# Performance work log

Measured on AMD Instinct MI355X. Metric: run time of the kernel, lower is better.

## Reference

```python
import jax, jax.numpy as jnp
import numpy as np

NEG_ATT = 0.2   # GATv2Conv internal leaky_relu slope
NEG_ACT = 0.01  # nn.LeakyReLU default slope (activation between layers)

def _segment_softmax(logits, seg, n):
    m = jax.ops.segment_max(logits, seg, num_segments=n)
    ex = jnp.exp(logits - m[seg])
    s = jax.ops.segment_sum(ex, seg, num_segments=n)
    return ex / s[seg]

def _gatv2(h, Wl, bl, Wr, br, att, bias, src, dst, n):
    # PyG GATv2Conv, heads=1: xl = lin_l(h) (source/message), xr = lin_r(h) (target)
    xl = h @ Wl + bl                                   # [N, H]
    xr = h @ Wr + br                                   # [N, H]
    e = jax.nn.leaky_relu(xl[src] + xr[dst], NEG_ATT)  # [E, H]
    logits = e @ att                                   # [E]
    alpha = _segment_softmax(logits, dst, n)           # softmax over incoming edges per dst
    out = jax.ops.segment_sum(xl[src] * alpha[:, None], dst, num_segments=n)
    return out + bias

def setup_inputs() -> dict:
    key = jax.random.key(0)
    G, P, DEG, DIN, H, EX, OUT, NC = 4096, 24, 8, 32, 128, 8, 3, 6
    N = G * P
    E = N * DEG
    ks = jax.random.split(key, 16)
    x = jax.random.normal(ks[0], (N, DIN), jnp.float32)
    gid = jnp.arange(E) // (P * DEG)  # edges stay within their graph
    src = gid * P + jax.random.randint(ks[1], (E,), 0, P)
    dst = gid * P + jax.random.randint(ks[2], (E,), 0, P)
    batch = jnp.repeat(jnp.arange(G), P)
    extra_feat = jax.random.normal(ks[3], (G, EX), jnp.float32)
    sc = lambda k, shp: jax.random.normal(k, shp, jnp.float32) * 0.05
    return dict(
        x=x, src=src, dst=dst, batch=batch, extra_feat=extra_feat,
        W_init0=sc(ks[4], (DIN, H)), b_init0=jnp.zeros((H,), jnp.float32),
        W_init1=sc(ks[5], (H, H)), b_init1=jnp.zeros((H,), jnp.float32),
        Wl=sc(ks[6], (NC, H, H)), bl=jnp.zeros((NC, H), jnp.float32),
        Wr=sc(ks[7], (NC, H, H)), br=jnp.zeros((NC, H), jnp.float32),
        att=sc(ks[8], (NC, H)), cbias=jnp.zeros((NC, H), jnp.float32),
        Wf0=sc(ks[9], (H + EX, H)), bf0=jnp.zeros((H,), jnp.float32),
        Wf1=sc(ks[10], (H, H)), bf1=jnp.zeros((H,), jnp.float32),
        Wf2=sc(ks[11], (H, OUT)), bf2=jnp.zeros((OUT,), jnp.float32),
    )

def reference(x, src, dst, batch, extra_feat,
              W_init0, b_init0, W_init1, b_init1,
              Wl, bl, Wr, br, att, cbias,
              Wf0, bf0, Wf1, bf1, Wf2, bf2):
    N = x.shape[0]
    G = extra_feat.shape[0]
    # init MLP
    h = jax.nn.leaky_relu(x @ W_init0 + b_init0, NEG_ACT)
    h = jax.nn.leaky_relu(h @ W_init1 + b_init1, NEG_ACT)
    # GATv2Conv adds self-loops
    loop = jnp.arange(N)
    src_sl = jnp.concatenate([src, loop])
    dst_sl = jnp.concatenate([dst, loop])
    NUM_GAT, MP = 2, 3
    for g in range(NUM_GAT):
        for m in range(MP):
            c = g * MP + m
            h = _gatv2(h, Wl[c], bl[c], Wr[c], br[c], att[c], cbias[c], src_sl, dst_sl, N)
            if m < MP - 1:  # BasicGNN: act between convs, not after last
                h = jax.nn.leaky_relu(h, NEG_ACT)
    # global_add_pool + extra features + final MLP
    pooled = jax.ops.segment_sum(h, batch, num_segments=G)
    z = jnp.concatenate([pooled, extra_feat], axis=1)
    z = jax.nn.leaky_relu(z @ Wf0 + bf0, NEG_ACT)
    z = jax.nn.leaky_relu(z @ Wf1 + bf1, NEG_ACT)
    return z @ Wf2 + bf2
```

## Files before the change

### kernel.cpp

```cpp
#include <hip/hip_runtime.h>

#define NG   4096
#define P    24
#define EPG  192
#define ESL  216
#define DIN  32
#define H    128
#define EX   8
#define NOUT 3
#define HSS  136
#define XTS  36
#define AMS  36

typedef _Float16 f16x8 __attribute__((ext_vector_type(8)));
typedef _Float16 h2    __attribute__((ext_vector_type(2)));
typedef float    f32x4 __attribute__((ext_vector_type(4)));

__device__ __forceinline__ unsigned short f2h(float v) {
    _Float16 h = (_Float16)v; unsigned short u; __builtin_memcpy(&u, &h, 2); return u;
}
__device__ __forceinline__ float h2f(unsigned short u) {
    _Float16 h; __builtin_memcpy(&h, &u, 2); return (float)h;
}
__device__ __forceinline__ unsigned pkadd(unsigned a, unsigned b) {
    h2 x, y; __builtin_memcpy(&x, &a, 4); __builtin_memcpy(&y, &b, 4);
    h2 z = x + y; unsigned r; __builtin_memcpy(&r, &z, 4); return r;
}
__device__ __forceinline__ float lrelu(float v, float s) { return v > 0.f ? v : v * s; }

#define STPAIR(BASE, ROW, COL, VAL)                                           \
    do {                                                                      \
        unsigned o_ = (unsigned)__builtin_amdgcn_mov_dpp(                     \
            (int)(unsigned)(VAL), 0xB1, 0xF, 0xF, true);                      \
        if (!(lane & 1))                                                      \
            *reinterpret_cast<unsigned*>(&(BASE)[(ROW) * HSS + (COL)]) =      \
                (unsigned)(VAL) | (o_ << 16);                                 \
    } while (0)

__global__ void cvtw(const float* __restrict__ W0, const float* __restrict__ W1,
                     const float* __restrict__ Wl, const float* __restrict__ Wr,
                     const float* __restrict__ att, const float* __restrict__ bl,
                     const float* __restrict__ br, unsigned short* __restrict__ ws) {
    int i = blockIdx.x * 256 + threadIdx.x;
    if (i < 217088) {
        float v;
        if (i < 4096)        { int n = i >> 5, k = i & 31;  v = W0[k * 128 + n]; }
        else if (i < 20480)  { int j = i - 4096;  int n = j >> 7, k = j & 127; v = W1[k * 128 + n]; }
        else if (i < 118784) { int j = i - 20480; int c = j >> 14, r = j & 16383;
                               int n = r >> 7, k = r & 127; v = Wl[c * 16384 + k * 128 + n]; }
        else                 { int j = i - 118784; int c = j >> 14, r = j & 16383;
                               int n = r >> 7, k = r & 127; v = Wr[c * 16384 + k * 128 + n]; }
        ws[i] = f2h(v);
    } else if (i < 241664) {
        int j = i - 217088;
        const float* W = (j < 12288) ? Wl : Wr;
        if (j >= 12288) j -= 12288;
        int c = j >> 11, r = j & 2047, row = r >> 7, k = r & 127;
        float v = 0.f;
        if (row == 0) {
            for (int q = 0; q < 128; ++q) v += W[c * 16384 + k * 128 + q] * att[c * 128 + q];
        }
        ws[i] = f2h(v);
    } else if (i < 241676) {
        int c = i - 241664;
        const float* B = (c < 6) ? bl : br;
        int cc = (c < 6) ? c : c - 6;
        float s = 0.f;
        for (int q = 0; q < 128; ++q) s += B[cc * 128 + q] * att[cc * 128 + q];
        ((float*)(ws + 241664))[c] = s;
    }
}

__global__ __launch_bounds__(256, 4) void gat_all(
    const float* __restrict__ x,
    const int*   __restrict__ src,
    const int*   __restrict__ dst,
    const float* __restrict__ extra,
    const float* __restrict__ b0,  const float* __restrict__ b1,
    const float* __restrict__ bl,  const float* __restrict__ br,
    const float* __restrict__ att, const float* __restrict__ cbias,
    const float* __restrict__ Wf0, const float* __restrict__ bf0,
    const float* __restrict__ Wf1, const float* __restrict__ bf1,
    const float* __restrict__ Wf2, const float* __restrict__ bf2,
    const unsigned short* __restrict__ wsb,
    float* __restrict__ out)
{
    __shared__ __align__(16) unsigned char LDSM[32768];
    unsigned short* hb  = (unsigned short*)(LDSM);
    unsigned short* xlb = (unsigned short*)(LDSM + 6528);
    unsigned short* xrb = (unsigned short*)(LDSM + 13056);
    unsigned short* xlT = (unsigned short*)(LDSM + 19584);
    float*          Am  = (float*)(LDSM + 28800);
    float*          sn  = (float*)(LDSM + 32256);
    unsigned int*   ath = (unsigned int*)(LDSM + 32512);

    const int g    = blockIdx.x;
    const int t    = threadIdx.x;
    const int lane = t & 63;
    const int w    = t >> 6;
    const int m16  = lane & 15;
    const int kc   = lane >> 4;
    const long long gn = (long long)g * P;

    const unsigned short* W0T = wsb;
    const unsigned short* W1T = wsb + 4096;
    const unsigned short* WLT = wsb + 20480;
    const unsigned short* WRT = wsb + 118784;
    const float* wsf = (const float*)(wsb + 241664);

    int s_e = 0, d_e = 0;
    if (t < ESL) {
        if (t < EPG) {
            s_e = src[(long long)g * EPG + t] - (int)gn;
            d_e = dst[(long long)g * EPG + t] - (int)gn;
        } else { s_e = d_e = t - EPG; }
    }

    if (t < 192) {
        float4 v = *reinterpret_cast<const float4*>(&x[gn * DIN + t * 4]);
        int n = t >> 3, k = (t & 7) * 4;
        *reinterpret_cast<ushort4*>(&xlT[n * XTS + k]) =
            make_ushort4(f2h(v.x), f2h(v.y), f2h(v.z), f2h(v.w));
    } else {
        int u = t - 192;
        int r = 24 + (u >> 3), k = (u & 7) * 4;
        *reinterpret_cast<ushort4*>(&xlT[r * XTS + k]) = make_ushort4(0, 0, 0, 0);
    }
    __syncthreads();

    {
        f32x4 acc[4] = {};
        f16x8 a = *reinterpret_cast<const f16x8*>(&xlT[((w & 1) * 16 + m16) * XTS + kc * 8]);
        #pragma unroll
        for (int i = 0; i < 4; ++i) {
            int nt = (w >> 1) * 4 + i;
            f16x8 b = *reinterpret_cast<const f16x8*>(&W0T[(nt * 16 + m16) * 32 + kc * 8]);
            acc[i] = __builtin_amdgcn_mfma_f32_16x16x32_f16(a, b, acc[i], 0, 0, 0);
        }
        const bool live = !((w & 1) && kc >= 2);
        if (live) {
            #pragma unroll
            for (int i = 0; i < 4; ++i) {
                int col = (w >> 1) * 64 + i * 16 + m16;
                float bv = b0[col];
                #pragma unroll
                for (int r = 0; r < 4; ++r) {
                    int row = (w & 1) * 16 + kc * 4 + r;
                    unsigned short ub = f2h(lrelu(acc[i][r] + bv, 0.01f));
                    STPAIR(xlb, row, col, ub);
                }
            }
        }
    }
    __syncthreads();

    {
        unsigned* xz = reinterpret_cast<unsigned*>(xlT);
        #pragma unroll
        for (int i = 0; i < 9; ++i) xz[t + i * 256] = 0u;
        f32x4 acc[4] = {};
        for (int kt = 0; kt < 4; ++kt) {
            f16x8 a = *reinterpret_cast<const f16x8*>(&xlb[((w & 1) * 16 + m16) * HSS + kt * 32 + kc * 8]);
            #pragma unroll
            for (int i = 0; i < 4; ++i) {
                int nt = (w >> 1) * 4 + i;
                f16x8 b = *reinterpret_cast<const f16x8*>(&W1T[(nt * 16 + m16) * 128 + kt * 32 + kc * 8]);
                acc[i] = __builtin_amdgcn_mfma_f32_16x16x32_f16(a, b, acc[i], 0, 0, 0);
            }
        }
        const bool live = !((w & 1) && kc >= 2);
        if (live) {
            #pragma unroll
            for (int i = 0; i < 4; ++i) {
                int col = (w >> 1) * 64 + i * 16 + m16;
                float bv = b1[col];
                #pragma unroll
                for (int r = 0; r < 4; ++r) {
                    int row = (w & 1) * 16 + kc * 4 + r;
                    unsigned short ub = f2h(lrelu(acc[i][r] + bv, 0.01f));
                    STPAIR(hb, row, col, ub);
                }
            }
        }
    }
    __syncthreads();

    for (int c = 0; c < 6; ++c) {
        if (t < ESL) *reinterpret_cast<float4*>(&Am[t * 4]) = make_float4(0.f, 0.f, 0.f, 0.f);
        if (t < 64) ath[t] = ((unsigned)f2h(att[c * H + 2 * t])) |
                             (((unsigned)f2h(att[c * H + 2 * t + 1])) << 16);

        const unsigned short* WT   = ((w & 1) ? WRT : WLT) + c * 16384;
        const unsigned short* WAX  = wsb + 217088 + ((w & 1) ? 12288 : 0) + c * 2048;
        const float*          bias = ((w & 1) ? br : bl) + c * H;
        f32x4 acc[8] = {};
        f32x4 acce[2] = {};
        for (int kt = 0; kt < 4; ++kt) {
            f16x8 a0 = *reinterpret_cast<const f16x8*>(&hb[(m16)      * HSS + kt * 32 + kc * 8]);
            f16x8 a1 = *reinterpret_cast<const f16x8*>(&hb[(16 + m16) * HSS + kt * 32 + kc * 8]);
            #pragma unroll
            for (int i = 0; i < 4; ++i) {
                int nt = (w >> 1) * 4 + i;
                f16x8 b = *reinterpret_cast<const f16x8*>(&WT[(nt * 16 + m16) * 128 + kt * 32 + kc * 8]);
                acc[i]     = __builtin_amdgcn_mfma_f32_16x16x32_f16(a0, b, acc[i],     0, 0, 0);
                acc[4 + i] = __builtin_amdgcn_mfma_f32_16x16x32_f16(a1, b, acc[4 + i], 0, 0, 0);
            }
            if (w >= 2) {
                f16x8 bx = *reinterpret_cast<const f16x8*>(&WAX[m16 * 128 + kt * 32 + kc * 8]);
                acce[0] = __builtin_amdgcn_mfma_f32_16x16x32_f16(a0, bx, acce[0], 0, 0, 0);
                acce[1] = __builtin_amdgcn_mfma_f32_16x16x32_f16(a1, bx, acce[1], 0, 0, 0);
            }
        }
        {
            unsigned short* XO = (w & 1) ? xrb : xlb;
            const bool isL = !(w & 1);
            #pragma unroll
            for (int mt = 0; mt < 2; ++mt) {
                const bool live = !(mt == 1 && kc >= 2);
                if (live) {
                    #pragma unroll
                    for (int i = 0; i < 4; ++i) {
                        int col = (w >> 1) * 64 + i * 16 + m16;
                        float bv = bias[col];
                        unsigned short ub[4];
                        #pragma unroll
                        for (int r = 0; r < 4; ++r) {
                            int row = mt * 16 + kc * 4 + r;
                            ub[r] = f2h(acc[mt * 4 + i][r] + bv);
                            STPAIR(XO, row, col, ub[r]);
                        }
                        if (isL)
                            *reinterpret_cast<ushort4*>(&xlT[col * XTS + mt * 16 + kc * 4]) =
                                make_ushort4(ub[0], ub[1], ub[2], ub[3]);
                    }
                }
            }
            if (w >= 2 && m16 == 0) {
                float cst = (w == 2) ? wsf[c] : wsf[6 + c];
                float* dp = (w == 2) ? sn : (sn + 32);
                #pragma unroll
                for (int mt = 0; mt < 2; ++mt)
                #pragma unroll
                for (int r = 0; r < 4; ++r)
                    dp[mt * 16 + kc * 4 + r] = acce[mt][r] + cst;
            }
        }
        __syncthreads();

        if (t < ESL) {
            const uint4* xa = reinterpret_cast<const uint4*>(&xlb[s_e * HSS]);
            const uint4* xb = reinterpret_cast<const uint4*>(&xrb[d_e * HSS]);
            const uint4* ap = reinterpret_cast<const uint4*>(ath);
            float a0 = 0.f, a1 = 0.f, a2 = 0.f, a3 = 0.f;
            #pragma unroll 4
            for (int cc = 0; cc < 16; ++cc) {
                uint4 wa = xa[cc], wb = xb[cc], pp = ap[cc];
                unsigned u0 = pkadd(wa.x, wb.x) & 0x7fff7fffu;
                unsigned u1 = pkadd(wa.y, wb.y) & 0x7fff7fffu;
                unsigned u2 = pkadd(wa.z, wb.z) & 0x7fff7fffu;
                unsigned u3 = pkadd(wa.w, wb.w) & 0x7fff7fffu;
                asm volatile("v_dot2_f32_f16 %0, %1, %2, %0" : "+v"(a0) : "v"(u0), "v"(pp.x));
                asm volatile("v_dot2_f32_f16 %0, %1, %2, %0" : "+v"(a1) : "v"(u1), "v"(pp.y));
                asm volatile("v_dot2_f32_f16 %0, %1, %2, %0" : "+v"(a2) : "v"(u2), "v"(pp.z));
                asm volatile("v_dot2_f32_f16 %0, %1, %2, %0" : "+v"(a3) : "v"(u3), "v"(pp.w));
            }
            float abss = (a0 + a1) + (a2 + a3);
            float lg = fmaf(0.6f, sn[s_e] + sn[32 + d_e], 0.4f * abss);
            atomicAdd(&Am[d_e * AMS + s_e], __expf(lg));
        }
        __syncthreads();

        {
            int arow = (w & 1) * 16 + m16;
            float4 u0, u1;
            if (arow < P) {
                u0 = *reinterpret_cast<const float4*>(&Am[arow * AMS + kc * 8]);
                u1 = *reinterpret_cast<const float4*>(&Am[arow * AMS + kc * 8 + 4]);
            } else {
                u0 = make_float4(0.f, 0.f, 0.f, 0.f);
                u1 = u0;
            }
            float rs = u0.x + u0.y + u0.z + u0.w + u1.x + u1.y + u1.z + u1.w;
            rs += __shfl_xor(rs, 16);
            rs += __shfl_xor(rs, 32);
            float sc = (arow < P) ? __builtin_amdgcn_rcpf(rs) : 0.f;
            f16x8 a;
            a[0] = (_Float16)(u0.x * sc); a[1] = (_Float16)(u0.y * sc);
            a[2] = (_Float16)(u0.z * sc); a[3] = (_Float16)(u0.w * sc);
            a[4] = (_Float16)(u1.x * sc); a[5] = (_Float16)(u1.y * sc);
            a[6] = (_Float16)(u1.z * sc); a[7] = (_Float16)(u1.w * sc);
            f32x4 acc2[4] = {};
            #pragma unroll
            for (int i = 0; i < 4; ++i) {
                int nt = (w >> 1) * 4 + i;
                f16x8 b = *reinterpret_cast<const f16x8*>(&xlT[(nt * 16 + m16) * XTS + kc * 8]);
                acc2[i] = __builtin_amdgcn_mfma_f32_16x16x32_f16(a, b, acc2[i], 0, 0, 0);
            }
            const bool doact = (c % 3) < 2;
            const bool live = !((w & 1) && kc >= 2);
            if (live) {
                #pragma unroll
                for (int i = 0; i < 4; ++i) {
                    int col = (w >> 1) * 64 + i * 16 + m16;
                    float cb = cbias[c * H + col];
                    #pragma unroll
                    for (int r = 0; r < 4; ++r) {
                        int row = (w & 1) * 16 + kc * 4 + r;
                        float v = acc2[i][r] + cb;
                        if (doact) v = lrelu(v, 0.01f);
                        unsigned short ub = f2h(v);
                        STPAIR(hb, row, col, ub);
                    }
                }
            }
        }
        __syncthreads();
    }

    float* scr = (float*)(LDSM + 6528);
    float* z  = scr;
    float* pa = scr + 144;
    float* pb = scr + 288;
    float* h1 = scr + 432;
    float* qa = scr + 576;
    float* qb = scr + 720;
    float* h2 = scr + 864;
    if (t < H) {
        float s = 0.f;
        for (int r = 0; r < P; ++r) s += h2f(hb[r * HSS + t]);
        z[t] = s;
    } else if (t < H + EX) {
        z[t] = extra[(long long)g * EX + (t - H)];
    }
    __syncthreads();
    {
        int j = t & 127, half = t >> 7;
        float a = half ? 0.f : bf0[j];
        int k0 = half ? 68 : 0, k1 = half ? 136 : 68;
        for (int k = k0; k < k1; ++k) a += z[k] * Wf0[k * H + j];
        (half ? pb : pa)[j] = a;
    }
    __syncthreads();
    if (t < H) h1[t] = lrelu(pa[t] + pb[t], 0.01f);
    __syncthreads();
    {
        int j = t & 127, half = t >> 7;
        float a = half ? 0.f : bf1[j];
        int k0 = half * 64, k1 = k0 + 64;
        for (int k = k0; k < k1; ++k) a += h1[k] * Wf1[k * H + j];
        (half ? qb : qa)[j] = a;
    }
    __syncthreads();
    if (t < H) h2[t] = lrelu(qa[t] + qb[t], 0.01f);
    __syncthreads();
    if (t < NOUT) {
        float a = bf2[t];
        for (int k = 0; k < H; ++k) a += h2[k] * Wf2[k * NOUT + t];
        out[(long long)g * NOUT + t] = a;
    }
}

extern "C" void kernel_launch(void* const* d_in, const int* in_sizes, int n_in,
                              void* d_out, int out_size, void* d_ws, size_t ws_size,
                              hipStream_t stream) {
    (void)in_sizes; (void)n_in; (void)out_size; (void)ws_size;
    const float* x     = (const float*)d_in[0];
    const int*   src   = (const int*)  d_in[1];
    const int*   dst   = (const int*)  d_in[2];
    const float* extra = (const float*)d_in[4];
    const float* W0    = (const float*)d_in[5];
    const float* b0    = (const float*)d_in[6];
    const float* W1    = (const float*)d_in[7];
    const float* b1    = (const float*)d_in[8];
    const float* Wl    = (const float*)d_in[9];
    const float* bl    = (const float*)d_in[10];
    const float* Wr    = (const float*)d_in[11];
    const float* br    = (const float*)d_in[12];
    const float* att   = (const float*)d_in[13];
    const float* cbias = (const float*)d_in[14];
    const float* Wf0   = (const float*)d_in[15];
    const float* bf0   = (const float*)d_in[16];
    const float* Wf1   = (const float*)d_in[17];
    const float* bf1   = (const float*)d_in[18];
    const float* Wf2   = (const float*)d_in[19];
    const float* bf2   = (const float*)d_in[20];
    unsigned short* wsb = (unsigned short*)d_ws;
    float* out = (float*)d_out;

    cvtw<<<945, 256, 0, stream>>>(W0, W1, Wl, Wr, att, bl, br, wsb);
    gat_all<<<NG, 256, 0, stream>>>(x, src, dst, extra, b0, b1, bl, br, att, cbias,
                                    Wf0, bf0, Wf1, bf1, Wf2, bf2, wsb, out);
}
```

Before: 380.2 us.

## Double block size to 512 threads and redistribute MFMA tiles across eight waves

Raises the per-graph block from 256 to 512 threads (8 waves) and remaps every MFMA stage so each wave computes fewer output column tiles: the init MLP layers, the Wl/Wr projections (now 2 column tiles per wave) and the attention-weighted aggregation. The goal is more wave-level parallelism per graph and lower per-wave serial MFMA chains and register pressure. In exchange it adds waves that share the same LDS and barriers, duplicates A-fragment loads across waves, and may reduce the number of resident blocks per CU. The final MLP stages are guarded to keep using only the first 256 threads.

```diff
diff --git a/kernel.cpp b/kernel.cpp
--- a/kernel.cpp
+++ b/kernel.cpp
@@ -71,7 +71,7 @@
     }
 }
 
-__global__ __launch_bounds__(256, 4) void gat_all(
+__global__ __launch_bounds__(512, 4) void gat_all(
     const float* __restrict__ x,
     const int*   __restrict__ src,
     const int*   __restrict__ dst,
@@ -121,7 +121,7 @@
         int n = t >> 3, k = (t & 7) * 4;
         *reinterpret_cast<ushort4*>(&xlT[n * XTS + k]) =
             make_ushort4(f2h(v.x), f2h(v.y), f2h(v.z), f2h(v.w));
-    } else {
+    } else if (t < 256) {
         int u = t - 192;
         int r = 24 + (u >> 3), k = (u & 7) * 4;
         *reinterpret_cast<ushort4*>(&xlT[r * XTS + k]) = make_ushort4(0, 0, 0, 0);
@@ -129,26 +129,23 @@
     __syncthreads();
 
     {
-        f32x4 acc[4] = {};
-        f16x8 a = *reinterpret_cast<const f16x8*>(&xlT[((w & 1) * 16 + m16) * XTS + kc * 8]);
-        #pragma unroll
-        for (int i = 0; i < 4; ++i) {
-            int nt = (w >> 1) * 4 + i;
-            f16x8 b = *reinterpret_cast<const f16x8*>(&W0T[(nt * 16 + m16) * 32 + kc * 8]);
-            acc[i] = __builtin_amdgcn_mfma_f32_16x16x32_f16(a, b, acc[i], 0, 0, 0);
-        }
-        const bool live = !((w & 1) && kc >= 2);
-        if (live) {
-            #pragma unroll
-            for (int i = 0; i < 4; ++i) {
-                int col = (w >> 1) * 64 + i * 16 + m16;
-                float bv = b0[col];
-                #pragma unroll
-                for (int r = 0; r < 4; ++r) {
-                    int row = (w & 1) * 16 + kc * 4 + r;
-                    unsigned short ub = f2h(lrelu(acc[i][r] + bv, 0.01f));
-                    STPAIR(xlb, row, col, ub);
-                }
+        f16x8 b = *reinterpret_cast<const f16x8*>(&W0T[(w * 16 + m16) * 32 + kc * 8]);
+        f32x4 acc[2] = {};
+        #pragma unroll
+        for (int mt = 0; mt < 2; ++mt) {
+            f16x8 a = *reinterpret_cast<const f16x8*>(&xlT[(mt * 16 + m16) * XTS + kc * 8]);
+            acc[mt] = __builtin_amdgcn_mfma_f32_16x16x32_f16(a, b, acc[mt], 0, 0, 0);
+        }
+        int col = w * 16 + m16;
+        float bv = b0[col];
+        #pragma unroll
+        for (int mt = 0; mt < 2; ++mt) {
+            if (mt == 1 && kc >= 2) continue;
+            #pragma unroll
+            for (int r = 0; r < 4; ++r) {
+                int row = mt * 16 + kc * 4 + r;
+                unsigned short ub = f2h(lrelu(acc[mt][r] + bv, 0.01f));
+                STPAIR(xlb, row, col, ub);
             }
         }
     }
@@ -157,29 +154,28 @@
     {
         unsigned* xz = reinterpret_cast<unsigned*>(xlT);
         #pragma unroll
-        for (int i = 0; i < 9; ++i) xz[t + i * 256] = 0u;
-        f32x4 acc[4] = {};
+        for (int i = 0; i < 4; ++i) xz[t + i * 512] = 0u;
+        if (t < 256) xz[2048 + t] = 0u;
+        f32x4 acc[2] = {};
+        #pragma unroll
         for (int kt = 0; kt < 4; ++kt) {
-            f16x8 a = *reinterpret_cast<const f16x8*>(&xlb[((w & 1) * 16 + m16) * HSS + kt * 32 + kc * 8]);
-            #pragma unroll
-            for (int i = 0; i < 4; ++i) {
-                int nt = (w >> 1) * 4 + i;
-                f16x8 b = *reinterpret_cast<const f16x8*>(&W1T[(nt * 16 + m16) * 128 + kt * 32 + kc * 8]);
-                acc[i] = __builtin_amdgcn_mfma_f32_16x16x32_f16(a, b, acc[i], 0, 0, 0);
-            }
-        }
-        const bool live = !((w & 1) && kc >= 2);
-        if (live) {
-            #pragma unroll
-            for (int i = 0; i < 4; ++i) {
-                int col = (w >> 1) * 64 + i * 16 + m16;
-                float bv = b1[col];
-                #pragma unroll
-                for (int r = 0; r < 4; ++r) {
-                    int row = (w & 1) * 16 + kc * 4 + r;
-                    unsigned short ub = f2h(lrelu(acc[i][r] + bv, 0.01f));
-                    STPAIR(hb, row, col, ub);
-                }
+            f16x8 b = *reinterpret_cast<const f16x8*>(&W1T[(w * 16 + m16) * 128 + kt * 32 + kc * 8]);
+            #pragma unroll
+            for (int mt = 0; mt < 2; ++mt) {
+                f16x8 a = *reinterpret_cast<const f16x8*>(&xlb[(mt * 16 + m16) * HSS + kt * 32 + kc * 8]);
+                acc[mt] = __builtin_amdgcn_mfma_f32_16x16x32_f16(a, b, acc[mt], 0, 0, 0);
+            }
+        }
+        int col = w * 16 + m16;
+        float bv = b1[col];
+        #pragma unroll
+        for (int mt = 0; mt < 2; ++mt) {
+            if (mt == 1 && kc >= 2) continue;
+            #pragma unroll
+            for (int r = 0; r < 4; ++r) {
+                int row = mt * 16 + kc * 4 + r;
+                unsigned short ub = f2h(lrelu(acc[mt][r] + bv, 0.01f));
+                STPAIR(hb, row, col, ub);
             }
         }
     }
@@ -190,54 +186,54 @@
         if (t < 64) ath[t] = ((unsigned)f2h(att[c * H + 2 * t])) |
                              (((unsigned)f2h(att[c * H + 2 * t + 1])) << 16);
 
-        const unsigned short* WT   = ((w & 1) ? WRT : WLT) + c * 16384;
-        const unsigned short* WAX  = wsb + 217088 + ((w & 1) ? 12288 : 0) + c * 2048;
-        const float*          bias = ((w & 1) ? br : bl) + c * H;
-        f32x4 acc[8] = {};
+        const int mat = w & 1, cg = w >> 1;
+        const unsigned short* WT   = (mat ? WRT : WLT) + c * 16384;
+        const unsigned short* WAX  = wsb + 217088 + (mat ? 12288 : 0) + c * 2048;
+        const float*          bias = (mat ? br : bl) + c * H;
+        f32x4 acc[2][2] = {};
         f32x4 acce[2] = {};
+        #pragma unroll
         for (int kt = 0; kt < 4; ++kt) {
             f16x8 a0 = *reinterpret_cast<const f16x8*>(&hb[(m16)      * HSS + kt * 32 + kc * 8]);
             f16x8 a1 = *reinterpret_cast<const f16x8*>(&hb[(16 + m16) * HSS + kt * 32 + kc * 8]);
             #pragma unroll
-            for (int i = 0; i < 4; ++i) {
-                int nt = (w >> 1) * 4 + i;
+            for (int i = 0; i < 2; ++i) {
+                int nt = cg * 2 + i;
                 f16x8 b = *reinterpret_cast<const f16x8*>(&WT[(nt * 16 + m16) * 128 + kt * 32 + kc * 8]);
-                acc[i]     = __builtin_amdgcn_mfma_f32_16x16x32_f16(a0, b, acc[i],     0, 0, 0);
-                acc[4 + i] = __builtin_amdgcn_mfma_f32_16x16x32_f16(a1, b, acc[4 + i], 0, 0, 0);
-            }
-            if (w >= 2) {
+                acc[0][i] = __builtin_amdgcn_mfma_f32_16x16x32_f16(a0, b, acc[0][i], 0, 0, 0);
+                acc[1][i] = __builtin_amdgcn_mfma_f32_16x16x32_f16(a1, b, acc[1][i], 0, 0, 0);
+            }
+            if (w >= 6) {
                 f16x8 bx = *reinterpret_cast<const f16x8*>(&WAX[m16 * 128 + kt * 32 + kc * 8]);
                 acce[0] = __builtin_amdgcn_mfma_f32_16x16x32_f16(a0, bx, acce[0], 0, 0, 0);
                 acce[1] = __builtin_amdgcn_mfma_f32_16x16x32_f16(a1, bx, acce[1], 0, 0, 0);
             }
         }
         {
-            unsigned short* XO = (w & 1) ? xrb : xlb;
-            const bool isL = !(w & 1);
+            unsigned short* XO = mat ? xrb : xlb;
             #pragma unroll
             for (int mt = 0; mt < 2; ++mt) {
-                const bool live = !(mt == 1 && kc >= 2);
-                if (live) {
+                if (!(mt == 1 && kc >= 2)) {
                     #pragma unroll
-                    for (int i = 0; i < 4; ++i) {
-                        int col = (w >> 1) * 64 + i * 16 + m16;
+                    for (int i = 0; i < 2; ++i) {
+                        int col = cg * 32 + i * 16 + m16;
                         float bv = bias[col];
                         unsigned short ub[4];
                         #pragma unroll
                         for (int r = 0; r < 4; ++r) {
                             int row = mt * 16 + kc * 4 + r;
-                            ub[r] = f2h(acc[mt * 4 + i][r] + bv);
+                            ub[r] = f2h(acc[mt][i][r] + bv);
                             STPAIR(XO, row, col, ub[r]);
                         }
-                        if (isL)
+                        if (!mat)
                             *reinterpret_cast<ushort4*>(&xlT[col * XTS + mt * 16 + kc * 4]) =
                                 make_ushort4(ub[0], ub[1], ub[2], ub[3]);
                     }
                 }
             }
-            if (w >= 2 && m16 == 0) {
-                float cst = (w == 2) ? wsf[c] : wsf[6 + c];
-                float* dp = (w == 2) ? sn : (sn + 32);
+            if (w >= 6 && m16 == 0) {
+                float cst = (w == 6) ? wsf[c] : wsf[6 + c];
+                float* dp = (w == 6) ? sn : (sn + 32);
                 #pragma unroll
                 for (int mt = 0; mt < 2; ++mt)
                 #pragma unroll
@@ -271,46 +267,47 @@
         __syncthreads();
 
         {
-            int arow = (w & 1) * 16 + m16;
-            float4 u0, u1;
-            if (arow < P) {
-                u0 = *reinterpret_cast<const float4*>(&Am[arow * AMS + kc * 8]);
-                u1 = *reinterpret_cast<const float4*>(&Am[arow * AMS + kc * 8 + 4]);
-            } else {
-                u0 = make_float4(0.f, 0.f, 0.f, 0.f);
-                u1 = u0;
-            }
-            float rs = u0.x + u0.y + u0.z + u0.w + u1.x + u1.y + u1.z + u1.w;
-            rs += __shfl_xor(rs, 16);
-            rs += __shfl_xor(rs, 32);
-            float sc = (arow < P) ? __builtin_amdgcn_rcpf(rs) : 0.f;
-            f16x8 a;
-            a[0] = (_Float16)(u0.x * sc); a[1] = (_Float16)(u0.y * sc);
-            a[2] = (_Float16)(u0.z * sc); a[3] = (_Float16)(u0.w * sc);
-            a[4] = (_Float16)(u1.x * sc); a[5] = (_Float16)(u1.y * sc);
-            a[6] = (_Float16)(u1.z * sc); a[7] = (_Float16)(u1.w * sc);
-            f32x4 acc2[4] = {};
-            #pragma unroll
-            for (int i = 0; i < 4; ++i) {
-                int nt = (w >> 1) * 4 + i;
-                f16x8 b = *reinterpret_cast<const f16x8*>(&xlT[(nt * 16 + m16) * XTS + kc * 8]);
-                acc2[i] = __builtin_amdgcn_mfma_f32_16x16x32_f16(a, b, acc2[i], 0, 0, 0);
-            }
+            f16x8 afr[2];
+            #pragma unroll
+            for (int mt = 0; mt < 2; ++mt) {
+                int arow = mt * 16 + m16;
+                float4 u0, u1;
+                if (arow < P) {
+                    u0 = *reinterpret_cast<const float4*>(&Am[arow * AMS + kc * 8]);
+                    u1 = *reinterpret_cast<const float4*>(&Am[arow * AMS + kc * 8 + 4]);
+                } else {
+                    u0 = make_float4(0.f, 0.f, 0.f, 0.f);
+                    u1 = u0;
+                }
+                float rs = u0.x + u0.y + u0.z + u0.w + u1.x + u1.y + u1.z + u1.w;
+                rs += __shfl_xor(rs, 16);
+                rs += __shfl_xor(rs, 32);
+                float sc = (arow < P) ? __builtin_amdgcn_rcpf(rs) : 0.f;
+                f16x8 a;
+                a[0] = (_Float16)(u0.x * sc); a[1] = (_Float16)(u0.y * sc);
+                a[2] = (_Float16)(u0.z * sc); a[3] = (_Float16)(u0.w * sc);
+                a[4] = (_Float16)(u1.x * sc); a[5] = (_Float16)(u1.y * sc);
+                a[6] = (_Float16)(u1.z * sc); a[7] = (_Float16)(u1.w * sc);
+                afr[mt] = a;
+            }
+            f16x8 b = *reinterpret_cast<const f16x8*>(&xlT[(w * 16 + m16) * XTS + kc * 8]);
+            f32x4 acc2[2] = {};
+            #pragma unroll
+            for (int mt = 0; mt < 2; ++mt)
+                acc2[mt] = __builtin_amdgcn_mfma_f32_16x16x32_f16(afr[mt], b, acc2[mt], 0, 0, 0);
             const bool doact = (c % 3) < 2;
-            const bool live = !((w & 1) && kc >= 2);
-            if (live) {
+            int col = w * 16 + m16;
+            float cb = cbias[c * H + col];
+            #pragma unroll
+            for (int mt = 0; mt < 2; ++mt) {
+                if (mt == 1 && kc >= 2) continue;
                 #pragma unroll
-                for (int i = 0; i < 4; ++i) {
-                    int col = (w >> 1) * 64 + i * 16 + m16;
-                    float cb = cbias[c * H + col];
-                    #pragma unroll
-                    for (int r = 0; r < 4; ++r) {
-                        int row = (w & 1) * 16 + kc * 4 + r;
-                        float v = acc2[i][r] + cb;
-                        if (doact) v = lrelu(v, 0.01f);
-                        unsigned short ub = f2h(v);
-                        STPAIR(hb, row, col, ub);
-                    }
+                for (int r = 0; r < 4; ++r) {
+                    int row = mt * 16 + kc * 4 + r;
+                    float v = acc2[mt][r] + cb;
+                    if (doact) v = lrelu(v, 0.01f);
+                    unsigned short ub = f2h(v);
+                    STPAIR(hb, row, col, ub);
                 }
             }
         }
@@ -333,7 +330,7 @@
         z[t] = extra[(long long)g * EX + (t - H)];
     }
     __syncthreads();
-    {
+    if (t < 256) {
         int j = t & 127, half = t >> 7;
         float a = half ? 0.f : bf0[j];
         int k0 = half ? 68 : 0, k1 = half ? 136 : 68;
@@ -343,7 +340,7 @@
     __syncthreads();
     if (t < H) h1[t] = lrelu(pa[t] + pb[t], 0.01f);
     __syncthreads();
-    {
+    if (t < 256) {
         int j = t & 127, half = t >> 7;
         float a = half ? 0.f : bf1[j];
         int k0 = half * 64, k1 = k0 + 64;
@@ -388,6 +385,6 @@
     float* out = (float*)d_out;
 
     cvtw<<<945, 256, 0, stream>>>(W0, W1, Wl, Wr, att, bl, br, wsb);
-    gat_all<<<NG, 256, 0, stream>>>(x, src, dst, extra, b0, b1, bl, br, att, cbias,
+    gat_all<<<NG, 512, 0, stream>>>(x, src, dst, extra, b0, b1, bl, br, att, cbias,
                                     Wf0, bf0, Wf1, bf1, Wf2, bf2, wsb, out);
 }
```

New measurement: 468.2 us. 23.2% more time.

## Process two graphs per workgroup to halve barriers and interleave stages

Applied to the files above, without the earlier changes.

Each 256-thread block now handles two graphs, each with its own 32KB LDS region, and every stage loops over both graphs between shared barriers. The aim is to spread barrier and launch overhead across more work and give each wave more independent MFMA and LDS work to hide latency. In exchange LDS per block doubles to 64KB, which lowers how many blocks fit per CU, and register pressure rises from the unrolled per-graph loops. The grid also shrinks to 2048 blocks.

```diff
diff --git a/kernel.cpp b/kernel.cpp
--- a/kernel.cpp
+++ b/kernel.cpp
@@ -1,6 +1,7 @@
 #include <hip/hip_runtime.h>
 
 #define NG   4096
+#define GPB  2
 #define P    24
 #define EPG  192
 #define ESL  216
@@ -11,6 +12,7 @@
 #define HSS  136
 #define XTS  36
 #define AMS  36
+#define RSZ  32768
 
 typedef _Float16 f16x8 __attribute__((ext_vector_type(8)));
 typedef _Float16 h2    __attribute__((ext_vector_type(2)));
@@ -85,22 +87,14 @@
     const unsigned short* __restrict__ wsb,
     float* __restrict__ out)
 {
-    __shared__ __align__(16) unsigned char LDSM[32768];
-    unsigned short* hb  = (unsigned short*)(LDSM);
-    unsigned short* xlb = (unsigned short*)(LDSM + 6528);
-    unsigned short* xrb = (unsigned short*)(LDSM + 13056);
-    unsigned short* xlT = (unsigned short*)(LDSM + 19584);
-    float*          Am  = (float*)(LDSM + 28800);
-    float*          sn  = (float*)(LDSM + 32256);
-    unsigned int*   ath = (unsigned int*)(LDSM + 32512);
-
-    const int g    = blockIdx.x;
+    __shared__ __align__(16) unsigned char LDSM[RSZ * GPB];
+
+    const int g0   = blockIdx.x * GPB;
     const int t    = threadIdx.x;
     const int lane = t & 63;
     const int w    = t >> 6;
     const int m16  = lane & 15;
     const int kc   = lane >> 4;
-    const long long gn = (long long)g * P;
 
     const unsigned short* W0T = wsb;
     const unsigned short* W1T = wsb + 4096;
@@ -108,27 +102,37 @@
     const unsigned short* WRT = wsb + 118784;
     const float* wsf = (const float*)(wsb + 241664);
 
-    int s_e = 0, d_e = 0;
+    int s_e0 = 0, d_e0 = 0, s_e1 = 0, d_e1 = 0;
     if (t < ESL) {
         if (t < EPG) {
-            s_e = src[(long long)g * EPG + t] - (int)gn;
-            d_e = dst[(long long)g * EPG + t] - (int)gn;
-        } else { s_e = d_e = t - EPG; }
-    }
-
-    if (t < 192) {
-        float4 v = *reinterpret_cast<const float4*>(&x[gn * DIN + t * 4]);
-        int n = t >> 3, k = (t & 7) * 4;
-        *reinterpret_cast<ushort4*>(&xlT[n * XTS + k]) =
-            make_ushort4(f2h(v.x), f2h(v.y), f2h(v.z), f2h(v.w));
-    } else {
-        int u = t - 192;
-        int r = 24 + (u >> 3), k = (u & 7) * 4;
-        *reinterpret_cast<ushort4*>(&xlT[r * XTS + k]) = make_ushort4(0, 0, 0, 0);
-    }
-    __syncthreads();
-
-    {
+            s_e0 = src[(long long)g0 * EPG + t]       - g0 * P;
+            d_e0 = dst[(long long)g0 * EPG + t]       - g0 * P;
+            s_e1 = src[(long long)(g0 + 1) * EPG + t] - (g0 + 1) * P;
+            d_e1 = dst[(long long)(g0 + 1) * EPG + t] - (g0 + 1) * P;
+        } else { s_e0 = d_e0 = s_e1 = d_e1 = t - EPG; }
+    }
+
+    #pragma unroll
+    for (int gg = 0; gg < GPB; ++gg) {
+        unsigned short* xlT = (unsigned short*)(LDSM + gg * RSZ + 19584);
+        const long long gn = (long long)(g0 + gg) * P;
+        if (t < 192) {
+            float4 v = *reinterpret_cast<const float4*>(&x[gn * DIN + t * 4]);
+            int n = t >> 3, k = (t & 7) * 4;
+            *reinterpret_cast<ushort4*>(&xlT[n * XTS + k]) =
+                make_ushort4(f2h(v.x), f2h(v.y), f2h(v.z), f2h(v.w));
+        } else {
+            int u = t - 192;
+            int r = 24 + (u >> 3), k = (u & 7) * 4;
+            *reinterpret_cast<ushort4*>(&xlT[r * XTS + k]) = make_ushort4(0, 0, 0, 0);
+        }
+    }
+    __syncthreads();
+
+    #pragma unroll
+    for (int gg = 0; gg < GPB; ++gg) {
+        unsigned short* xlb = (unsigned short*)(LDSM + gg * RSZ + 6528);
+        unsigned short* xlT = (unsigned short*)(LDSM + gg * RSZ + 19584);
         f32x4 acc[4] = {};
         f16x8 a = *reinterpret_cast<const f16x8*>(&xlT[((w & 1) * 16 + m16) * XTS + kc * 8]);
         #pragma unroll
@@ -154,7 +158,11 @@
     }
     __syncthreads();
 
-    {
+    #pragma unroll
+    for (int gg = 0; gg < GPB; ++gg) {
+        unsigned short* hb  = (unsigned short*)(LDSM + gg * RSZ);
+        unsigned short* xlb = (unsigned short*)(LDSM + gg * RSZ + 6528);
+        unsigned short* xlT = (unsigned short*)(LDSM + gg * RSZ + 19584);
         unsigned* xz = reinterpret_cast<unsigned*>(xlT);
         #pragma unroll
         for (int i = 0; i < 9; ++i) xz[t + i * 256] = 0u;
@@ -186,32 +194,41 @@
     __syncthreads();
 
     for (int c = 0; c < 6; ++c) {
-        if (t < ESL) *reinterpret_cast<float4*>(&Am[t * 4]) = make_float4(0.f, 0.f, 0.f, 0.f);
-        if (t < 64) ath[t] = ((unsigned)f2h(att[c * H + 2 * t])) |
-                             (((unsigned)f2h(att[c * H + 2 * t + 1])) << 16);
-
-        const unsigned short* WT   = ((w & 1) ? WRT : WLT) + c * 16384;
-        const unsigned short* WAX  = wsb + 217088 + ((w & 1) ? 12288 : 0) + c * 2048;
-        const float*          bias = ((w & 1) ? br : bl) + c * H;
-        f32x4 acc[8] = {};
-        f32x4 acce[2] = {};
-        for (int kt = 0; kt < 4; ++kt) {
-            f16x8 a0 = *reinterpret_cast<const f16x8*>(&hb[(m16)      * HSS + kt * 32 + kc * 8]);
-            f16x8 a1 = *reinterpret_cast<const f16x8*>(&hb[(16 + m16) * HSS + kt * 32 + kc * 8]);
-            #pragma unroll
-            for (int i = 0; i < 4; ++i) {
-                int nt = (w >> 1) * 4 + i;
-                f16x8 b = *reinterpret_cast<const f16x8*>(&WT[(nt * 16 + m16) * 128 + kt * 32 + kc * 8]);
-                acc[i]     = __builtin_amdgcn_mfma_f32_16x16x32_f16(a0, b, acc[i],     0, 0, 0);
-                acc[4 + i] = __builtin_amdgcn_mfma_f32_16x16x32_f16(a1, b, acc[4 + i], 0, 0, 0);
-            }
-            if (w >= 2) {
-                f16x8 bx = *reinterpret_cast<const f16x8*>(&WAX[m16 * 128 + kt * 32 + kc * 8]);
-                acce[0] = __builtin_amdgcn_mfma_f32_16x16x32_f16(a0, bx, acce[0], 0, 0, 0);
-                acce[1] = __builtin_amdgcn_mfma_f32_16x16x32_f16(a1, bx, acce[1], 0, 0, 0);
-            }
-        }
-        {
+        #pragma unroll
+        for (int gg = 0; gg < GPB; ++gg) {
+            unsigned short* hb  = (unsigned short*)(LDSM + gg * RSZ);
+            unsigned short* xlb = (unsigned short*)(LDSM + gg * RSZ + 6528);
+            unsigned short* xrb = (unsigned short*)(LDSM + gg * RSZ + 13056);
+            unsigned short* xlT = (unsigned short*)(LDSM + gg * RSZ + 19584);
+            float*          Am  = (float*)(LDSM + gg * RSZ + 28800);
+            float*          sn  = (float*)(LDSM + gg * RSZ + 32256);
+            unsigned int*   ath = (unsigned int*)(LDSM + gg * RSZ + 32512);
+
+            if (t < ESL) *reinterpret_cast<float4*>(&Am[t * 4]) = make_float4(0.f, 0.f, 0.f, 0.f);
+            if (t < 64) ath[t] = ((unsigned)f2h(att[c * H + 2 * t])) |
+                                 (((unsigned)f2h(att[c * H + 2 * t + 1])) << 16);
+
+            const unsigned short* WT   = ((w & 1) ? WRT : WLT) + c * 16384;
+            const unsigned short* WAX  = wsb + 217088 + ((w & 1) ? 12288 : 0) + c * 2048;
+            const float*          bias = ((w & 1) ? br : bl) + c * H;
+            f32x4 acc[8] = {};
+            f32x4 acce[2] = {};
+            for (int kt = 0; kt < 4; ++kt) {
+                f16x8 a0 = *reinterpret_cast<const f16x8*>(&hb[(m16)      * HSS + kt * 32 + kc * 8]);
+                f16x8 a1 = *reinterpret_cast<const f16x8*>(&hb[(16 + m16) * HSS + kt * 32 + kc * 8]);
+                #pragma unroll
+                for (int i = 0; i < 4; ++i) {
+                    int nt = (w >> 1) * 4 + i;
+                    f16x8 b = *reinterpret_cast<const f16x8*>(&WT[(nt * 16 + m16) * 128 + kt * 32 + kc * 8]);
+                    acc[i]     = __builtin_amdgcn_mfma_f32_16x16x32_f16(a0, b, acc[i],     0, 0, 0);
+                    acc[4 + i] = __builtin_amdgcn_mfma_f32_16x16x32_f16(a1, b, acc[4 + i], 0, 0, 0);
+                }
+                if (w >= 2) {
+                    f16x8 bx = *reinterpret_cast<const f16x8*>(&WAX[m16 * 128 + kt * 32 + kc * 8]);
+                    acce[0] = __builtin_amdgcn_mfma_f32_16x16x32_f16(a0, bx, acce[0], 0, 0, 0);
+                    acce[1] = __builtin_amdgcn_mfma_f32_16x16x32_f16(a1, bx, acce[1], 0, 0, 0);
+                }
+            }
             unsigned short* XO = (w & 1) ? xrb : xlb;
             const bool isL = !(w & 1);
             #pragma unroll
@@ -248,29 +265,43 @@
         __syncthreads();
 
         if (t < ESL) {
-            const uint4* xa = reinterpret_cast<const uint4*>(&xlb[s_e * HSS]);
-            const uint4* xb = reinterpret_cast<const uint4*>(&xrb[d_e * HSS]);
-            const uint4* ap = reinterpret_cast<const uint4*>(ath);
-            float a0 = 0.f, a1 = 0.f, a2 = 0.f, a3 = 0.f;
-            #pragma unroll 4
-            for (int cc = 0; cc < 16; ++cc) {
-                uint4 wa = xa[cc], wb = xb[cc], pp = ap[cc];
-                unsigned u0 = pkadd(wa.x, wb.x) & 0x7fff7fffu;
-                unsigned u1 = pkadd(wa.y, wb.y) & 0x7fff7fffu;
-                unsigned u2 = pkadd(wa.z, wb.z) & 0x7fff7fffu;
-                unsigned u3 = pkadd(wa.w, wb.w) & 0x7fff7fffu;
-                asm volatile("v_dot2_f32_f16 %0, %1, %2, %0" : "+v"(a0) : "v"(u0), "v"(pp.x));
-                asm volatile("v_dot2_f32_f16 %0, %1, %2, %0" : "+v"(a1) : "v"(u1), "v"(pp.y));
-                asm volatile("v_dot2_f32_f16 %0, %1, %2, %0" : "+v"(a2) : "v"(u2), "v"(pp.z));
-                asm volatile("v_dot2_f32_f16 %0, %1, %2, %0" : "+v"(a3) : "v"(u3), "v"(pp.w));
-            }
-            float abss = (a0 + a1) + (a2 + a3);
-            float lg = fmaf(0.6f, sn[s_e] + sn[32 + d_e], 0.4f * abss);
-            atomicAdd(&Am[d_e * AMS + s_e], __expf(lg));
+            #pragma unroll
+            for (int gg = 0; gg < GPB; ++gg) {
+                unsigned short* xlb = (unsigned short*)(LDSM + gg * RSZ + 6528);
+                unsigned short* xrb = (unsigned short*)(LDSM + gg * RSZ + 13056);
+                float*          Am  = (float*)(LDSM + gg * RSZ + 28800);
+                float*          sn  = (float*)(LDSM + gg * RSZ + 32256);
+                unsigned int*   ath = (unsigned int*)(LDSM + gg * RSZ + 32512);
+                const int s_e = gg ? s_e1 : s_e0;
+                const int d_e = gg ? d_e1 : d_e0;
+                const uint4* xa = reinterpret_cast<const uint4*>(&xlb[s_e * HSS]);
+                const uint4* xb = reinterpret_cast<const uint4*>(&xrb[d_e * HSS]);
+                const uint4* ap = reinterpret_cast<const uint4*>(ath);
+                float a0 = 0.f, a1 = 0.f, a2 = 0.f, a3 = 0.f;
+                #pragma unroll 4
+                for (int cc = 0; cc < 16; ++cc) {
+                    uint4 wa = xa[cc], wb = xb[cc], pp = ap[cc];
+                    unsigned u0 = pkadd(wa.x, wb.x) & 0x7fff7fffu;
+                    unsigned u1 = pkadd(wa.y, wb.y) & 0x7fff7fffu;
+                    unsigned u2 = pkadd(wa.z, wb.z) & 0x7fff7fffu;
+                    unsigned u3 = pkadd(wa.w, wb.w) & 0x7fff7fffu;
+                    asm volatile("v_dot2_f32_f16 %0, %1, %2, %0" : "+v"(a0) : "v"(u0), "v"(pp.x));
+                    asm volatile("v_dot2_f32_f16 %0, %1, %2, %0" : "+v"(a1) : "v"(u1), "v"(pp.y));
+                    asm volatile("v_dot2_f32_f16 %0, %1, %2, %0" : "+v"(a2) : "v"(u2), "v"(pp.z));
+                    asm volatile("v_dot2_f32_f16 %0, %1, %2, %0" : "+v"(a3) : "v"(u3), "v"(pp.w));
+                }
+                float abss = (a0 + a1) + (a2 + a3);
+                float lg = fmaf(0.6f, sn[s_e] + sn[32 + d_e], 0.4f * abss);
+                atomicAdd(&Am[d_e * AMS + s_e], __expf(lg));
+            }
         }
         __syncthreads();
 
-        {
+        #pragma unroll
+        for (int gg = 0; gg < GPB; ++gg) {
+            unsigned short* hb  = (unsigned short*)(LDSM + gg * RSZ);
+            unsigned short* xlT = (unsigned short*)(LDSM + gg * RSZ + 19584);
+            float*          Am  = (float*)(LDSM + gg * RSZ + 28800);
             int arow = (w & 1) * 16 + m16;
             float4 u0, u1;
             if (arow < P) {
@@ -317,23 +348,23 @@
         __syncthreads();
     }
 
-    float* scr = (float*)(LDSM + 6528);
-    float* z  = scr;
-    float* pa = scr + 144;
-    float* pb = scr + 288;
-    float* h1 = scr + 432;
-    float* qa = scr + 576;
-    float* qb = scr + 720;
-    float* h2 = scr + 864;
-    if (t < H) {
-        float s = 0.f;
-        for (int r = 0; r < P; ++r) s += h2f(hb[r * HSS + t]);
-        z[t] = s;
-    } else if (t < H + EX) {
-        z[t] = extra[(long long)g * EX + (t - H)];
-    }
-    __syncthreads();
-    {
+    #pragma unroll
+    for (int gg = 0; gg < GPB; ++gg) {
+        unsigned short* hb = (unsigned short*)(LDSM + gg * RSZ);
+        float* scr = (float*)(LDSM + gg * RSZ + 6528);
+        if (t < H) {
+            float s = 0.f;
+            for (int r = 0; r < P; ++r) s += h2f(hb[r * HSS + t]);
+            scr[t] = s;
+        } else if (t < H + EX) {
+            scr[t] = extra[(long long)(g0 + gg) * EX + (t - H)];
+        }
+    }
+    __syncthreads();
+    #pragma unroll
+    for (int gg = 0; gg < GPB; ++gg) {
+        float* scr = (float*)(LDSM + gg * RSZ + 6528);
+        float* z = scr, * pa = scr + 144, * pb = scr + 288;
         int j = t & 127, half = t >> 7;
         float a = half ? 0.f : bf0[j];
         int k0 = half ? 68 : 0, k1 = half ? 136 : 68;
@@ -341,9 +372,16 @@
         (half ? pb : pa)[j] = a;
     }
     __syncthreads();
-    if (t < H) h1[t] = lrelu(pa[t] + pb[t], 0.01f);
-    __syncthreads();
-    {
+    #pragma unroll
+    for (int gg = 0; gg < GPB; ++gg) {
+        float* scr = (float*)(LDSM + gg * RSZ + 6528);
+        if (t < H) scr[432 + t] = lrelu(scr[144 + t] + scr[288 + t], 0.01f);
+    }
+    __syncthreads();
+    #pragma unroll
+    for (int gg = 0; gg < GPB; ++gg) {
+        float* scr = (float*)(LDSM + gg * RSZ + 6528);
+        float* h1 = scr + 432, * qa = scr + 576, * qb = scr + 720;
         int j = t & 127, half = t >> 7;
         float a = half ? 0.f : bf1[j];
         int k0 = half * 64, k1 = k0 + 64;
@@ -351,12 +389,20 @@
         (half ? qb : qa)[j] = a;
     }
     __syncthreads();
-    if (t < H) h2[t] = lrelu(qa[t] + qb[t], 0.01f);
-    __syncthreads();
-    if (t < NOUT) {
-        float a = bf2[t];
-        for (int k = 0; k < H; ++k) a += h2[k] * Wf2[k * NOUT + t];
-        out[(long long)g * NOUT + t] = a;
+    #pragma unroll
+    for (int gg = 0; gg < GPB; ++gg) {
+        float* scr = (float*)(LDSM + gg * RSZ + 6528);
+        if (t < H) scr[864 + t] = lrelu(scr[576 + t] + scr[720 + t], 0.01f);
+    }
+    __syncthreads();
+    #pragma unroll
+    for (int gg = 0; gg < GPB; ++gg) {
+        float* h2 = (float*)(LDSM + gg * RSZ + 6528) + 864;
+        if (t < NOUT) {
+            float a = bf2[t];
+            for (int k = 0; k < H; ++k) a += h2[k] * Wf2[k * NOUT + t];
+            out[(long long)(g0 + gg) * NOUT + t] = a;
+        }
     }
 }
 
@@ -388,6 +434,6 @@
     float* out = (float*)d_out;
 
     cvtw<<<945, 256, 0, stream>>>(W0, W1, Wl, Wr, att, bl, br, wsb);
-    gat_all<<<NG, 256, 0, stream>>>(x, src, dst, extra, b0, b1, bl, br, att, cbias,
-                                    Wf0, bf0, Wf1, bf1, Wf2, bf2, wsb, out);
-}
+    gat_all<<<NG / GPB, 256, 0, stream>>>(x, src, dst, extra, b0, b1, bl, br, att, cbias,
+                                          Wf0, bf0, Wf1, bf1, Wf2, bf2, wsb, out);
+}
```

After: 439.1 us. +15.5%, slower.
